# Performance work log

Measured on AMD Instinct MI355X. Metric: run time of the kernel, lower is better.

The kernel has to match this reference:

```python
import jax, jax.numpy as jnp
import numpy as np

DIM = 2048
DIM_HEAD = 128
HEADS = 16
FF_INNER = 4 * DIM  # 8192
ATTN_INNER = DIM_HEAD * HEADS  # 2048
FUSED_DIMS = (ATTN_INNER, DIM_HEAD, DIM_HEAD, FF_INNER * 2)
R = 8
B, N = 2, 2048


def setup_inputs() -> dict:
    key = jax.random.key(0)
    ks = jax.random.split(key, 12)
    s = 0.02
    return {
        "x": jax.random.normal(ks[0], (B, N, DIM), jnp.float32),
        "gamma": jnp.ones((DIM,), jnp.float32),
        "w_fused": jax.random.normal(ks[1], (DIM, sum(FUSED_DIMS)), jnp.float32) * s,
        "w_attn_out": jax.random.normal(ks[2], (ATTN_INNER, DIM), jnp.float32) * s,
        "w_ff_out": jax.random.normal(ks[3], (FF_INNER, DIM), jnp.float32) * s,
        "a_q": jax.random.normal(ks[4], (DIM, R), jnp.float32) * s,
        "b_q": jax.random.normal(ks[5], (R, ATTN_INNER), jnp.float32) * s,
        "a_k": jax.random.normal(ks[6], (DIM, R), jnp.float32) * s,
        "b_k": jax.random.normal(ks[7], (R, DIM_HEAD), jnp.float32) * s,
        "a_v": jax.random.normal(ks[8], (DIM, R), jnp.float32) * s,
        "b_v": jax.random.normal(ks[9], (R, DIM_HEAD), jnp.float32) * s,
        "a_o": jax.random.normal(ks[10], (ATTN_INNER, R), jnp.float32) * s,
        "b_o": jax.random.normal(ks[11], (R, DIM), jnp.float32) * s,
    }


def _rotate_half(t):
    t1, t2 = jnp.split(t, 2, axis=-1)
    return jnp.concatenate((-t2, t1), axis=-1)


def _rope(pos, t):
    return t * jnp.cos(pos) + _rotate_half(t) * jnp.sin(pos)


def reference(x, gamma, w_fused, w_attn_out, w_ff_out,
              a_q, b_q, a_k, b_k, a_v, b_v, a_o, b_o):
    b, n, d = x.shape
    # LayerNorm (beta buffer is zeros)
    mu = jnp.mean(x, -1, keepdims=True)
    var = jnp.var(x, -1, keepdims=True)
    xn = (x - mu) * jax.lax.rsqrt(var + 1e-5) * gamma

    proj = xn @ w_fused
    splits = np.cumsum(FUSED_DIMS)[:-1]
    q, k, v, ff = jnp.split(proj, splits, axis=-1)

    # fused QKV LoRA (scale alpha/r = 1)
    q = q + (xn @ a_q) @ b_q
    k = k + (xn @ a_k) @ b_k
    v = v + (xn @ a_v) @ b_v

    q = q.reshape(b, n, HEADS, DIM_HEAD).transpose(0, 2, 1, 3)  # b h n d
    q = q * (DIM_HEAD ** -0.5)

    # rotary embedding
    inv_freq = 1.0 / (10000.0 ** (jnp.arange(0, DIM_HEAD, 2, dtype=jnp.float32) / DIM_HEAD))
    freqs = jnp.arange(n, dtype=jnp.float32)[:, None] * inv_freq[None, :]  # n, d/2
    pos = jnp.concatenate((freqs, freqs), axis=-1)  # n, d
    q = _rope(pos, q)          # broadcast over b,h
    k = _rope(pos, k)          # b n d (single head, MQA)

    sim = jnp.einsum('bhid,bjd->bhij', q, k)
    causal = jnp.triu(jnp.ones((n, n), dtype=bool), 1)
    sim = jnp.where(causal, -jnp.finfo(sim.dtype).max, sim)
    attn = jax.nn.softmax(sim, axis=-1)
    out = jnp.einsum('bhij,bjd->bhid', attn, v)
    out = out.transpose(0, 2, 1, 3).reshape(b, n, ATTN_INNER)

    attn_out = out @ w_attn_out + (out @ a_o) @ b_o

    x1, gate = jnp.split(ff, 2, axis=-1)
    ff_out = (jax.nn.silu(gate) * x1) @ w_ff_out
    return attn_out + ff_out
```

## Files before the change

### kernel.cpp

```cpp
#include <hip/hip_runtime.h>

typedef unsigned short u16;
typedef __attribute__((ext_vector_type(8))) short s8v;
typedef __attribute__((ext_vector_type(4))) short s4v;
typedef __attribute__((ext_vector_type(4))) float f32x4;

__device__ __forceinline__ u16 f2bf(float f) {
  unsigned int u = __float_as_uint(f);
  u += ((u >> 16) & 1u) + 0x7FFFu;
  return (u16)(u >> 16);
}
__device__ __forceinline__ float bf2f(u16 h) {
  return __uint_as_float(((unsigned int)h) << 16);
}
__device__ __forceinline__ void gl_lds16(const void* g, void* l) {
  __builtin_amdgcn_global_load_lds(
      (__attribute__((address_space(1))) void*)g,
      (__attribute__((address_space(3))) void*)l, 16, 0, 0);
}
__device__ __forceinline__ f32x4 mfma16(s8v a, s8v b, f32x4 c) {
  return __builtin_amdgcn_mfma_f32_16x16x32_bf16(a, b, c, 0, 0, 0);
}

__global__ void transpose_cvt(const float* __restrict__ in, u16* __restrict__ out,
                              int rows, int cols, int ldo) {
  __shared__ float tile[32][33];
  int c0 = blockIdx.x * 32, r0 = blockIdx.y * 32;
  int tx = threadIdx.x, ty = threadIdx.y;
#pragma unroll
  for (int i = 0; i < 4; i++)
    tile[ty + i * 8][tx] = in[(long)(r0 + ty + i * 8) * cols + c0 + tx];
  __syncthreads();
#pragma unroll
  for (int i = 0; i < 4; i++)
    out[(long)(c0 + ty + i * 8) * ldo + r0 + tx] = f2bf(tile[tx][ty + i * 8]);
}

__global__ void vtrans(const u16* __restrict__ proj, u16* __restrict__ v_t) {
  __shared__ u16 tile[32][33];
  int n0 = blockIdx.x * 32, d0 = blockIdx.y * 32, b = blockIdx.z;
  int tx = threadIdx.x, ty = threadIdx.y;
#pragma unroll
  for (int i = 0; i < 4; i++)
    tile[ty + i * 8][tx] =
        proj[((long)b * 2048 + n0 + ty + i * 8) * 18688 + 2176 + d0 + tx];
  __syncthreads();
#pragma unroll
  for (int i = 0; i < 4; i++)
    v_t[((long)b * 128 + d0 + ty + i * 8) * 2048 + n0 + tx] = tile[tx][ty + i * 8];
}

__global__ void fill_aug_k(u16* __restrict__ wt, int N, int ldo, int naug,
                           const float* __restrict__ bq, const float* __restrict__ bk,
                           const float* __restrict__ bv) {
  long idx = (long)blockIdx.x * 256 + threadIdx.x;
  if (idx >= (long)N * naug) return;
  int n = (int)(idx / naug), j = (int)(idx % naug);
  float v = 0.f;
  if (bq && j < 8 && n < 2048) v = bq[j * 2048 + n];
  else if (bk && j >= 8 && j < 16 && n >= 2048 && n < 2176) v = bk[(j - 8) * 128 + (n - 2048)];
  else if (bv && j >= 16 && j < 24 && n >= 2176 && n < 2304) v = bv[(j - 16) * 128 + (n - 2176)];
  wt[(long)n * ldo + 2048 + j] = f2bf(v);
}

__global__ __launch_bounds__(256) void layernorm_k(const float* __restrict__ x,
                                                   const float* __restrict__ gamma,
                                                   u16* __restrict__ xn) {
  const int row = blockIdx.x, tid = threadIdx.x;
  const float* xr = x + (long)row * 2048 + tid * 8;
  float4 v0 = *(const float4*)xr;
  float4 v1 = *(const float4*)(xr + 4);
  float vals[8] = {v0.x, v0.y, v0.z, v0.w, v1.x, v1.y, v1.z, v1.w};
  float s = 0.f, q = 0.f;
#pragma unroll
  for (int e = 0; e < 8; e++) { s += vals[e]; q += vals[e] * vals[e]; }
#pragma unroll
  for (int off = 32; off > 0; off >>= 1) {
    s += __shfl_down(s, off, 64);
    q += __shfl_down(q, off, 64);
  }
  __shared__ float red[8];
  const int w = tid >> 6, lane = tid & 63;
  if (lane == 0) { red[w] = s; red[4 + w] = q; }
  __syncthreads();
  if (tid == 0) {
    float S = red[0] + red[1] + red[2] + red[3];
    float Q = red[4] + red[5] + red[6] + red[7];
    float mu = S * (1.f / 2048.f);
    float var = Q * (1.f / 2048.f) - mu * mu;
    red[0] = mu; red[1] = rsqrtf(var + 1e-5f);
  }
  __syncthreads();
  float mu = red[0], rs = red[1];
  const float* g = gamma + tid * 8;
  u16 ov[8];
#pragma unroll
  for (int e = 0; e < 8; e++) ov[e] = f2bf((vals[e] - mu) * rs * g[e]);
  *(s8v*)(xn + (long)row * 2112 + tid * 8) = *(const s8v*)ov;
}

__global__ __launch_bounds__(256) void lora_down_x(u16* __restrict__ xn_aug,
                                                   const float* __restrict__ aq,
                                                   const float* __restrict__ ak,
                                                   const float* __restrict__ av) {
  const int row = blockIdx.x, tid = threadIdx.x;
  s8v xv = *(const s8v*)(xn_aug + (long)row * 2112 + tid * 8);
  float acc[3][8];
#pragma unroll
  for (int m = 0; m < 3; m++)
#pragma unroll
    for (int j = 0; j < 8; j++) acc[m][j] = 0.f;
  const float* mats[3] = {aq, ak, av};
#pragma unroll
  for (int e = 0; e < 8; e++) {
    float xe = bf2f((u16)xv[e]);
    int k = tid * 8 + e;
#pragma unroll
    for (int m = 0; m < 3; m++) {
      const float4* ap = (const float4*)(mats[m] + (long)k * 8);
      float4 a0 = ap[0], a1 = ap[1];
      acc[m][0] += xe * a0.x; acc[m][1] += xe * a0.y;
      acc[m][2] += xe * a0.z; acc[m][3] += xe * a0.w;
      acc[m][4] += xe * a1.x; acc[m][5] += xe * a1.y;
      acc[m][6] += xe * a1.z; acc[m][7] += xe * a1.w;
    }
  }
#pragma unroll
  for (int m = 0; m < 3; m++)
#pragma unroll
    for (int j = 0; j < 8; j++)
#pragma unroll
      for (int off = 32; off > 0; off >>= 1)
        acc[m][j] += __shfl_down(acc[m][j], off, 64);
  __shared__ float red[4][24];
  const int w = tid >> 6, lane = tid & 63;
  if (lane == 0)
    for (int m = 0; m < 3; m++)
      for (int j = 0; j < 8; j++) red[w][m * 8 + j] = acc[m][j];
  __syncthreads();
  if (tid < 64) {
    float v = 0.f;
    if (tid < 24) v = red[0][tid] + red[1][tid] + red[2][tid] + red[3][tid];
    xn_aug[(long)row * 2112 + 2048 + tid] = f2bf(v);
  }
}

__global__ __launch_bounds__(256) void lora_down_ctx(u16* __restrict__ ctx_aug,
                                                     const float* __restrict__ ao) {
  const int row = blockIdx.x, tid = threadIdx.x;
  s8v xv = *(const s8v*)(ctx_aug + (long)row * 2080 + tid * 8);
  float acc[8];
#pragma unroll
  for (int j = 0; j < 8; j++) acc[j] = 0.f;
#pragma unroll
  for (int e = 0; e < 8; e++) {
    float xe = bf2f((u16)xv[e]);
    int k = tid * 8 + e;
    const float4* ap = (const float4*)(ao + (long)k * 8);
    float4 a0 = ap[0], a1 = ap[1];
    acc[0] += xe * a0.x; acc[1] += xe * a0.y; acc[2] += xe * a0.z; acc[3] += xe * a0.w;
    acc[4] += xe * a1.x; acc[5] += xe * a1.y; acc[6] += xe * a1.z; acc[7] += xe * a1.w;
  }
#pragma unroll
  for (int j = 0; j < 8; j++)
#pragma unroll
    for (int off = 32; off > 0; off >>= 1)
      acc[j] += __shfl_down(acc[j], off, 64);
  __shared__ float red[4][8];
  const int w = tid >> 6, lane = tid & 63;
  if (lane == 0)
    for (int j = 0; j < 8; j++) red[w][j] = acc[j];
  __syncthreads();
  if (tid < 32) {
    float v = 0.f;
    if (tid < 8) v = red[0][tid] + red[1][tid] + red[2][tid] + red[3][tid];
    ctx_aug[(long)row * 2080 + 2048 + tid] = f2bf(v);
  }
}

__global__ void rope_k(u16* __restrict__ proj) {
  int idx = blockIdx.x * 256 + threadIdx.x;
  int i = idx & 63;
  int u = (idx >> 6) % 17;
  int row = idx / (17 * 64);
  int n = row & 2047;
  float invf = __powf(10000.f, -(float)i * (1.f / 64.f));
  float ang = (float)n * invf;
  float cs = cosf(ang), sn = sinf(ang);
  int cb = (u < 16) ? u * 128 : 2048;
  u16* p = proj + (long)row * 18688 + cb + i;
  float t1 = bf2f(p[0]), t2 = bf2f(p[64]);
  float sc = (u < 16) ? 0.08838834764831845f : 1.f;
  p[0]  = f2bf((t1 * cs - t2 * sn) * sc);
  p[64] = f2bf((t2 * cs + t1 * sn) * sc);
}

__global__ void silu_mul_k(u16* __restrict__ proj) {
  long idx = (long)blockIdx.x * 256 + threadIdx.x;
  int row = (int)(idx >> 10);
  int c8 = (int)(idx & 1023) * 8;
  u16* px = proj + (long)row * 18688 + 2304 + c8;
  const u16* pg = proj + (long)row * 18688 + 10496 + c8;
  s8v xv = *(const s8v*)px;
  s8v gv = *(const s8v*)pg;
  u16 ov[8];
#pragma unroll
  for (int e = 0; e < 8; e++) {
    float x1 = bf2f((u16)xv[e]);
    float g = bf2f((u16)gv[e]);
    ov[e] = f2bf(x1 * g / (1.f + __expf(-g)));
  }
  *(s8v*)px = *(const s8v*)ov;
}

__global__ __launch_bounds__(512, 2) void gemm256_bt(const u16* __restrict__ A,
                                                     const u16* __restrict__ Bt,
                                                     u16* __restrict__ C) {
  __shared__ u16 sh[4 * 16384];
  const int cpx = gridDim.x >> 3;
  const int swz = (blockIdx.x & 7) * cpx + (blockIdx.x >> 3);
  const int bm = swz & 15;
  const int bn = swz >> 4;
  const int tid = threadIdx.x;
  const int w = tid >> 6, lane = tid & 63;
  const int quad = lane >> 4, l15 = lane & 15;
  const int wm = w >> 2, wn = w & 3;
  const int rseg = (quad ^ ((l15 >> 1) & 3)) * 8;
  const int aoff = (wm * 128 + l15) * 32 + rseg;
  const int boff = (wn * 64 + l15) * 32 + rseg;
  const int srow = lane >> 2;
  const int sseg = ((lane & 3) ^ ((lane >> 3) & 3)) * 8;
  const u16* aSrc = A + (long)(bm * 256 + w * 16 + srow) * 2112 + sseg;
  const u16* bSrc = Bt + (long)(bn * 256 + w * 16 + srow) * 2112 + sseg;

  f32x4 acc[8][4];
#pragma unroll
  for (int i = 0; i < 8; i++)
#pragma unroll
    for (int j = 0; j < 4; j++) acc[i][j] = {0.f, 0.f, 0.f, 0.f};

#pragma unroll
  for (int t = 0; t < 3; t++) {
    gl_lds16(aSrc + t * 32, sh + t * 16384 + w * 512);
    gl_lds16(bSrc + t * 32, sh + t * 16384 + 8192 + w * 512);
    gl_lds16(aSrc + 128L * 2112 + t * 32, sh + t * 16384 + 4096 + w * 512);
    gl_lds16(bSrc + 128L * 2112 + t * 32, sh + t * 16384 + 8192 + 4096 + w * 512);
  }
  asm volatile("s_waitcnt vmcnt(8)" ::: "memory");
  __builtin_amdgcn_s_barrier();

  s8v bf[4];
  int kcol = 96;

#define STAGE_UNIT(NB, MH)                                                    \
  gl_lds16(aSrc + (MH) * (128L * 2112) + kcol,                                \
           sh + (NB) * 16384 + (MH) * 4096 + w * 512);                        \
  gl_lds16(bSrc + (MH) * (128L * 2112) + kcol,                                \
           sh + (NB) * 16384 + 8192 + (MH) * 4096 + w * 512);

#define PHASE(CUR, MH, DOB, STG, VM)                                          \
  {                                                                           \
    const u16* Ab = sh + (CUR) * 16384 + aoff + (MH) * 2048;                  \
    s8v af0 = *(const s8v*)(Ab);                                              \
    s8v af1 = *(const s8v*)(Ab + 512);                                        \
    s8v af2 = *(const s8v*)(Ab + 1024);                                       \
    s8v af3 = *(const s8v*)(Ab + 1536);                                       \
    if (DOB) {                                                                \
      const u16* Bb = sh + (CUR) * 16384 + 8192 + boff;                       \
      bf[0] = *(const s8v*)(Bb);                                              \
      bf[1] = *(const s8v*)(Bb + 512);                                        \
      bf[2] = *(const s8v*)(Bb + 1024);                                       \
      bf[3] = *(const s8v*)(Bb + 1536);                                       \
    }                                                                         \
    if (STG) { STAGE_UNIT((((CUR) + 3) & 3), MH) }                            \
    __builtin_amdgcn_s_setprio(1);                                            \
    _Pragma("unroll") for (int ni = 0; ni < 4; ni++) {                        \
      acc[(MH) * 4 + 0][ni] = mfma16(bf[ni], af0, acc[(MH) * 4 + 0][ni]);     \
      acc[(MH) * 4 + 1][ni] = mfma16(bf[ni], af1, acc[(MH) * 4 + 1][ni]);     \
      acc[(MH) * 4 + 2][ni] = mfma16(bf[ni], af2, acc[(MH) * 4 + 2][ni]);     \
      acc[(MH) * 4 + 3][ni] = mfma16(bf[ni], af3, acc[(MH) * 4 + 3][ni]);     \
    }                                                                         \
    __builtin_amdgcn_s_setprio(0);                                            \
    if ((VM) == 8) asm volatile("s_waitcnt vmcnt(8)" ::: "memory");           \
    if ((VM) == 4) asm volatile("s_waitcnt vmcnt(4)" ::: "memory");           \
    if ((VM) == 0) asm volatile("s_waitcnt vmcnt(0)" ::: "memory");           \
    if ((VM) != -1) __builtin_amdgcn_s_barrier();                             \
  }

#define TILE(CUR, STG, VM)       \
  PHASE(CUR, 0, 1, STG, -1)      \
  PHASE(CUR, 1, 0, STG, VM)      \
  kcol += 32;

  for (int t4 = 0; t4 < 15; t4++) {
    TILE(0, 1, 8)
    TILE(1, 1, 8)
    TILE(2, 1, 8)
    TILE(3, 1, 8)
  }
  TILE(0, 1, 8)
  TILE(1, 1, 8)
  TILE(2, 1, 8)
  TILE(3, 0, 4)
  TILE(0, 0, 0)
  TILE(1, 0, -1)

#undef TILE
#undef PHASE
#undef STAGE_UNIT

  const long m0 = (long)bm * 256 + wm * 128;
  const long n0 = (long)bn * 256 + wn * 64;
#pragma unroll
  for (int mi = 0; mi < 8; mi++) {
    long row = m0 + mi * 16 + l15;
#pragma unroll
    for (int ni = 0; ni < 4; ni++) {
      long col = n0 + ni * 16 + quad * 4;
      s4v pk = {(short)f2bf(acc[mi][ni][0]), (short)f2bf(acc[mi][ni][1]),
                (short)f2bf(acc[mi][ni][2]), (short)f2bf(acc[mi][ni][3])};
      *(s4v*)(C + row * 18688 + col) = pk;
    }
  }
}

enum { STORE_F32 = 1, ADD_F32 = 2 };
template <int MODE>
__global__ __launch_bounds__(512, 1) void gemm_out(const u16* __restrict__ A, int lda,
                                                   const u16* __restrict__ Bt, int ldb,
                                                   float* __restrict__ Cv, int ldc, int K) {
  __shared__ u16 sh[4 * 12288];
  const int cpx = gridDim.x >> 3;
  const int swz = (blockIdx.x & 7) * cpx + (blockIdx.x >> 3);
  const int bm = swz & 31;
  const int bn = swz >> 5;
  const int tid = threadIdx.x;
  const int w = tid >> 6, lane = tid & 63;
  const int quad = lane >> 4, l15 = lane & 15;
  const int wm = w >> 2, wn = w & 3;
  const int rseg = (quad ^ ((l15 >> 1) & 3)) * 8;
  const int aoff = (wm * 64 + l15) * 32 + rseg;
  const int boff = 4096 + (wn * 64 + l15) * 32 + rseg;
  const int srow = lane >> 2;
  const int sseg = ((lane & 3) ^ ((lane >> 3) & 3)) * 8;
  const u16* aSrc = A + (long)(bm * 128 + w * 16 + srow) * lda + sseg;
  const u16* bSrc0 = Bt + (long)(bn * 256 + w * 16 + srow) * ldb + sseg;
  const u16* bSrc1 = Bt + (long)(bn * 256 + 128 + w * 16 + srow) * ldb + sseg;
  const int NT = K >> 5;

  f32x4 acc[4][4];
#pragma unroll
  for (int i = 0; i < 4; i++)
#pragma unroll
    for (int j = 0; j < 4; j++) acc[i][j] = {0.f, 0.f, 0.f, 0.f};

#pragma unroll
  for (int t = 0; t < 3; t++) {
    gl_lds16(aSrc + t * 32, sh + t * 12288 + w * 512);
    gl_lds16(bSrc0 + t * 32, sh + t * 12288 + 4096 + w * 512);
    gl_lds16(bSrc1 + t * 32, sh + t * 12288 + 8192 + w * 512);
  }
  asm volatile("s_waitcnt vmcnt(6)" ::: "memory");
  __builtin_amdgcn_s_barrier();

  int kcol = 96;
  for (int t = 0; t < NT; ++t) {
    const int cur = (t & 3) * 12288;
    const u16* Ab = sh + cur + aoff;
    const u16* Bb = sh + cur + boff;
    s8v af[4], bf[4];
#pragma unroll
    for (int mi = 0; mi < 4; mi++) af[mi] = *(const s8v*)(Ab + mi * 512);
#pragma unroll
    for (int ni = 0; ni < 4; ni++) bf[ni] = *(const s8v*)(Bb + ni * 512);
    if (t < NT - 3) {
      const int nb = ((t + 3) & 3) * 12288;
      gl_lds16(aSrc + kcol, sh + nb + w * 512);
      gl_lds16(bSrc0 + kcol, sh + nb + 4096 + w * 512);
      gl_lds16(bSrc1 + kcol, sh + nb + 8192 + w * 512);
      kcol += 32;
    }
    __builtin_amdgcn_s_setprio(1);
#pragma unroll
    for (int mi = 0; mi < 4; mi++)
#pragma unroll
      for (int ni = 0; ni < 4; ni++)
        acc[mi][ni] = mfma16(bf[ni], af[mi], acc[mi][ni]);
    __builtin_amdgcn_s_setprio(0);
    if (t < NT - 3)       asm volatile("s_waitcnt vmcnt(6)" ::: "memory");
    else if (t == NT - 3) asm volatile("s_waitcnt vmcnt(3)" ::: "memory");
    else if (t == NT - 2) asm volatile("s_waitcnt vmcnt(0)" ::: "memory");
    if (t != NT - 1) __builtin_amdgcn_s_barrier();
  }

  const long m0 = (long)bm * 128 + wm * 64;
  const long n0 = (long)bn * 256 + wn * 64;
#pragma unroll
  for (int mi = 0; mi < 4; mi++) {
    long row = m0 + mi * 16 + l15;
#pragma unroll
    for (int ni = 0; ni < 4; ni++) {
      long col = n0 + ni * 16 + quad * 4;
      float* p = Cv + row * ldc + col;
      if (MODE == STORE_F32) {
        *(f32x4*)p = acc[mi][ni];
      } else {
        f32x4 old = *(const f32x4*)p;
        old += acc[mi][ni];
        *(f32x4*)p = old;
      }
    }
  }
}

__global__ __launch_bounds__(256) void flash_k(const u16* __restrict__ proj,
                                               const u16* __restrict__ v_t,
                                               u16* __restrict__ ctx) {
  __shared__ u16 Kt[4 * 1024];
  __shared__ u16 Vx[8 * 512];
  __shared__ u16 Pw[4 * 512];
  const int qt = blockIdx.x, h = blockIdx.y, b = blockIdx.z;
  const int tid = threadIdx.x;
  const int w = tid >> 6, lane = tid & 63, quad = lane >> 4, l15 = lane & 15;
  const int qbase = qt * 64 + w * 16;

  s8v qf[4];
  {
    long rowQ = (long)b * 2048 + qbase + l15;
    const u16* qp = proj + rowQ * 18688 + h * 128 + quad * 8;
#pragma unroll
    for (int kk = 0; kk < 4; kk++) qf[kk] = *(const s8v*)(qp + kk * 32);
  }
  f32x4 o[8];
#pragma unroll
  for (int i = 0; i < 8; i++) o[i] = {0.f, 0.f, 0.f, 0.f};
  float m_i[4] = {-1e30f, -1e30f, -1e30f, -1e30f};
  float l_i[4] = {0.f, 0.f, 0.f, 0.f};

  const int srow = lane >> 2;
  const int sseg = ((lane & 3) ^ ((lane >> 3) & 3)) * 8;
  const int rseg = (quad ^ ((l15 >> 1) & 3)) * 8;

  const int nkb = 2 * qt + 2;
  for (int kb = 0; kb < nkb; kb++) {
    const int k0 = kb * 32;
    {
      long rK = (long)b * 2048 + k0;
#pragma unroll
      for (int h2 = 0; h2 < 2; h2++)
        gl_lds16(proj + (rK + h2 * 16 + srow) * 18688 + 2048 + w * 32 + sseg,
                 Kt + w * 1024 + h2 * 512);
#pragma unroll
      for (int h2 = 0; h2 < 2; h2++)
        gl_lds16(v_t + ((long)b * 128 + w * 32 + h2 * 16 + srow) * 2048 + k0 + sseg,
                 Vx + (w * 2 + h2) * 512);
    }
    __syncthreads();
    if (k0 <= qbase + 15) {
      f32x4 s[2];
#pragma unroll
      for (int ni = 0; ni < 2; ni++) {
        f32x4 a = {0.f, 0.f, 0.f, 0.f};
#pragma unroll
        for (int kk = 0; kk < 4; kk++) {
          s8v kf = *(const s8v*)(Kt + kk * 1024 + (ni * 16 + l15) * 32 + rseg);
          a = mfma16(qf[kk], kf, a);
        }
        s[ni] = a;
      }
#pragma unroll
      for (int ni = 0; ni < 2; ni++) {
        int kg = k0 + ni * 16 + l15;
#pragma unroll
        for (int r = 0; r < 4; r++)
          if (kg > qbase + quad * 4 + r) s[ni][r] = -1e30f;
      }
      float al[4];
#pragma unroll
      for (int r = 0; r < 4; r++) {
        float mx = fmaxf(s[0][r], s[1][r]);
#pragma unroll
        for (int off = 8; off > 0; off >>= 1)
          mx = fmaxf(mx, __shfl_xor(mx, off, 16));
        float mn = fmaxf(m_i[r], mx);
        al[r] = __expf(m_i[r] - mn);
        m_i[r] = mn;
      }
#pragma unroll
      for (int ni = 0; ni < 2; ni++)
#pragma unroll
        for (int r = 0; r < 4; r++) s[ni][r] = __expf(s[ni][r] - m_i[r]);
#pragma unroll
      for (int r = 0; r < 4; r++) {
        float rs = s[0][r] + s[1][r];
#pragma unroll
        for (int off = 8; off > 0; off >>= 1)
          rs += __shfl_xor(rs, off, 16);
        l_i[r] = l_i[r] * al[r] + rs;
      }
#pragma unroll
      for (int ni = 0; ni < 2; ni++)
#pragma unroll
        for (int r = 0; r < 4; r++) {
          int p = quad * 4 + r;
          int sg = ni * 2 + (l15 >> 3);
          int sp = sg ^ ((p >> 1) & 3);
          Pw[w * 512 + p * 32 + sp * 8 + (l15 & 7)] = f2bf(s[ni][r]);
        }
      __asm__ volatile("s_waitcnt lgkmcnt(0)" ::: "memory");
#pragma unroll
      for (int nt = 0; nt < 8; nt++)
#pragma unroll
        for (int r = 0; r < 4; r++) o[nt][r] *= al[r];
      s8v pf = *(const s8v*)(Pw + w * 512 + l15 * 32 + rseg);
#pragma unroll
      for (int nt = 0; nt < 8; nt++) {
        s8v vf = *(const s8v*)(Vx + (nt * 16 + l15) * 32 + rseg);
        o[nt] = mfma16(pf, vf, o[nt]);
      }
    }
    __syncthreads();
  }
  float inv[4];
#pragma unroll
  for (int r = 0; r < 4; r++) inv[r] = 1.f / l_i[r];
#pragma unroll
  for (int nt = 0; nt < 8; nt++)
#pragma unroll
    for (int r = 0; r < 4; r++) {
      long row = (long)b * 2048 + qbase + quad * 4 + r;
      ctx[row * 2080 + h * 128 + nt * 16 + l15] = f2bf(o[nt][r] * inv[r]);
    }
}

#define OFF_WF   0L
#define OFF_WO   78938112L
#define OFF_WFF  87457792L
#define OFF_XN   121012224L
#define OFF_PROJ 138313728L
#define WS_NEED  291405824L

extern "C" void kernel_launch(void* const* d_in, const int* in_sizes, int n_in,
                              void* d_out, int out_size, void* d_ws, size_t ws_size,
                              hipStream_t stream) {
  const float* x       = (const float*)d_in[0];
  const float* gamma   = (const float*)d_in[1];
  const float* w_fused = (const float*)d_in[2];
  const float* w_attn  = (const float*)d_in[3];
  const float* w_ff    = (const float*)d_in[4];
  const float* a_q = (const float*)d_in[5];
  const float* b_q = (const float*)d_in[6];
  const float* a_k = (const float*)d_in[7];
  const float* b_k = (const float*)d_in[8];
  const float* a_v = (const float*)d_in[9];
  const float* b_v = (const float*)d_in[10];
  const float* a_o = (const float*)d_in[11];
  const float* b_o = (const float*)d_in[12];
  float* out = (float*)d_out;
  if (ws_size < (size_t)WS_NEED) return;

  char* ws = (char*)d_ws;
  u16* wf_t    = (u16*)(ws + OFF_WF);
  u16* ctx_aug = (u16*)(ws + OFF_WF);
  u16* wo_t    = (u16*)(ws + OFF_WO);
  u16* wff_t   = (u16*)(ws + OFF_WFF);
  u16* xn_aug  = (u16*)(ws + OFF_XN);
  u16* v_t     = (u16*)(ws + OFF_XN);
  u16* proj    = (u16*)(ws + OFF_PROJ);

  dim3 tb(32, 8);
  transpose_cvt<<<dim3(18688 / 32, 2048 / 32), tb, 0, stream>>>(w_fused, wf_t, 2048, 18688, 2112);
  transpose_cvt<<<dim3(2048 / 32, 2048 / 32), tb, 0, stream>>>(w_attn, wo_t, 2048, 2048, 2080);
  transpose_cvt<<<dim3(2048 / 32, 8192 / 32), tb, 0, stream>>>(w_ff, wff_t, 8192, 2048, 8192);
  fill_aug_k<<<(18688 * 64 + 255) / 256, 256, 0, stream>>>(wf_t, 18688, 2112, 64, b_q, b_k, b_v);
  fill_aug_k<<<(2048 * 32 + 255) / 256, 256, 0, stream>>>(wo_t, 2048, 2080, 32, b_o, nullptr, nullptr);

  layernorm_k<<<4096, 256, 0, stream>>>(x, gamma, xn_aug);
  lora_down_x<<<4096, 256, 0, stream>>>(xn_aug, a_q, a_k, a_v);

  gemm256_bt<<<dim3(16 * (18688 / 256)), 512, 0, stream>>>(xn_aug, wf_t, proj);

  rope_k<<<(4096 * 17 * 64) / 256, 256, 0, stream>>>(proj);
  silu_mul_k<<<(4096 * 1024) / 256, 256, 0, stream>>>(proj);
  vtrans<<<dim3(64, 4, 2), tb, 0, stream>>>(proj, v_t);

  flash_k<<<dim3(32, 16, 2), 256, 0, stream>>>(proj, v_t, ctx_aug);
  lora_down_ctx<<<4096, 256, 0, stream>>>(ctx_aug, a_o);

  gemm_out<STORE_F32><<<dim3(256), 512, 0, stream>>>(
      ctx_aug, 2080, wo_t, 2080, out, 2048, 2080);
  gemm_out<ADD_F32><<<dim3(256), 512, 0, stream>>>(
      proj + 2304, 18688, wff_t, 8192, out, 2048, 8192);
}
```

Baseline: 1.315 ms.

## Software-pipeline LDS fragment loads across k-tiles with double-buffered B registers

Restructures the main GEMM loop so the A fragments and B fragments for the next k-tile are read from LDS during the current tile's second MFMA half, using ping-pong B register buffers. It removes the mid-tile barrier point and changes the vmcnt waits to one barrier per tile with a deeper wait, so LDS read latency is hidden behind MFMA work. This raises register pressure and tightens the hazard window between the LDS buffer being refilled and being read. Correctness depends on the revised waitcnt and barrier placement.

```diff
diff --git a/kernel.cpp b/kernel.cpp
--- a/kernel.cpp
+++ b/kernel.cpp
@@ -246,68 +246,90 @@
     gl_lds16(aSrc + 128L * 2112 + t * 32, sh + t * 16384 + 4096 + w * 512);
     gl_lds16(bSrc + 128L * 2112 + t * 32, sh + t * 16384 + 8192 + 4096 + w * 512);
   }
-  asm volatile("s_waitcnt vmcnt(8)" ::: "memory");
+  asm volatile("s_waitcnt vmcnt(4)" ::: "memory");
   __builtin_amdgcn_s_barrier();
 
-  s8v bf[4];
+  s8v afc[4], afn[4], bfA[4], bfB[4];
+  {
+    const u16* Ab0 = sh + aoff;
+    afc[0] = *(const s8v*)(Ab0);
+    afc[1] = *(const s8v*)(Ab0 + 512);
+    afc[2] = *(const s8v*)(Ab0 + 1024);
+    afc[3] = *(const s8v*)(Ab0 + 1536);
+    const u16* Bb0 = sh + 8192 + boff;
+    bfA[0] = *(const s8v*)(Bb0);
+    bfA[1] = *(const s8v*)(Bb0 + 512);
+    bfA[2] = *(const s8v*)(Bb0 + 1024);
+    bfA[3] = *(const s8v*)(Bb0 + 1536);
+  }
+
   int kcol = 96;
 
-#define STAGE_UNIT(NB, MH)                                                    \
+#define STAGE_U(NB, MH)                                                       \
   gl_lds16(aSrc + (MH) * (128L * 2112) + kcol,                                \
            sh + (NB) * 16384 + (MH) * 4096 + w * 512);                        \
   gl_lds16(bSrc + (MH) * (128L * 2112) + kcol,                                \
            sh + (NB) * 16384 + 8192 + (MH) * 4096 + w * 512);
 
-#define PHASE(CUR, MH, DOB, STG, VM)                                          \
-  {                                                                           \
-    const u16* Ab = sh + (CUR) * 16384 + aoff + (MH) * 2048;                  \
-    s8v af0 = *(const s8v*)(Ab);                                              \
-    s8v af1 = *(const s8v*)(Ab + 512);                                        \
-    s8v af2 = *(const s8v*)(Ab + 1024);                                       \
-    s8v af3 = *(const s8v*)(Ab + 1536);                                       \
-    if (DOB) {                                                                \
-      const u16* Bb = sh + (CUR) * 16384 + 8192 + boff;                       \
-      bf[0] = *(const s8v*)(Bb);                                              \
-      bf[1] = *(const s8v*)(Bb + 512);                                        \
-      bf[2] = *(const s8v*)(Bb + 1024);                                       \
-      bf[3] = *(const s8v*)(Bb + 1536);                                       \
-    }                                                                         \
-    if (STG) { STAGE_UNIT((((CUR) + 3) & 3), MH) }                            \
+#define TILE(CUR, BFC, BFN, STG, RA, VM)                                      \
+  {                \
+    const u16* Abn = sh + (CUR) * 16384 + aoff + 2048;                        \
+    afn[0] = *(const s8v*)(Abn);                                              \
+    afn[1] = *(const s8v*)(Abn + 512);                                        \
+    afn[2] = *(const s8v*)(Abn + 1024);                                       \
+    afn[3] = *(const s8v*)(Abn + 1536);                                       \
+    if (STG) { STAGE_U((((CUR) + 3) & 3), 0) }                                \
     __builtin_amdgcn_s_setprio(1);                                            \
     _Pragma("unroll") for (int ni = 0; ni < 4; ni++) {                        \
-      acc[(MH) * 4 + 0][ni] = mfma16(bf[ni], af0, acc[(MH) * 4 + 0][ni]);     \
-      acc[(MH) * 4 + 1][ni] = mfma16(bf[ni], af1, acc[(MH) * 4 + 1][ni]);     \
-      acc[(MH) * 4 + 2][ni] = mfma16(bf[ni], af2, acc[(MH) * 4 + 2][ni]);     \
-      acc[(MH) * 4 + 3][ni] = mfma16(bf[ni], af3, acc[(MH) * 4 + 3][ni]);     \
+      acc[0][ni] = mfma16(BFC[ni], afc[0], acc[0][ni]);                       \
+      acc[1][ni] = mfma16(BFC[ni], afc[1], acc[1][ni]);                       \
+      acc[2][ni] = mfma16(BFC[ni], afc[2], acc[2][ni]);                       \
+      acc[3][ni] = mfma16(BFC[ni], afc[3], acc[3][ni]);                       \
     }                                                                         \
     __builtin_amdgcn_s_setprio(0);                                            \
-    if ((VM) == 8) asm volatile("s_waitcnt vmcnt(8)" ::: "memory");           \
+       \
+    if (RA) {                                                                 \
+      const u16* Abc = sh + (((CUR) + 1) & 3) * 16384 + aoff;                 \
+      afc[0] = *(const s8v*)(Abc);                                            \
+      afc[1] = *(const s8v*)(Abc + 512);                                      \
+      afc[2] = *(const s8v*)(Abc + 1024);                                     \
+      afc[3] = *(const s8v*)(Abc + 1536);                                     \
+      const u16* Bbn = sh + (((CUR) + 1) & 3) * 16384 + 8192 + boff;          \
+      BFN[0] = *(const s8v*)(Bbn);                                            \
+      BFN[1] = *(const s8v*)(Bbn + 512);                                      \
+      BFN[2] = *(const s8v*)(Bbn + 1024);                                     \
+      BFN[3] = *(const s8v*)(Bbn + 1536);                                     \
+    }                                                                         \
+    if (STG) { STAGE_U((((CUR) + 3) & 3), 1) }                                \
+    __builtin_amdgcn_s_setprio(1);                                            \
+    _Pragma("unroll") for (int ni = 0; ni < 4; ni++) {                        \
+      acc[4][ni] = mfma16(BFC[ni], afn[0], acc[4][ni]);                       \
+      acc[5][ni] = mfma16(BFC[ni], afn[1], acc[5][ni]);                       \
+      acc[6][ni] = mfma16(BFC[ni], afn[2], acc[6][ni]);                       \
+      acc[7][ni] = mfma16(BFC[ni], afn[3], acc[7][ni]);                       \
+    }                                                                         \
+    __builtin_amdgcn_s_setprio(0);                                            \
     if ((VM) == 4) asm volatile("s_waitcnt vmcnt(4)" ::: "memory");           \
     if ((VM) == 0) asm volatile("s_waitcnt vmcnt(0)" ::: "memory");           \
     if ((VM) != -1) __builtin_amdgcn_s_barrier();                             \
-  }
-
-#define TILE(CUR, STG, VM)       \
-  PHASE(CUR, 0, 1, STG, -1)      \
-  PHASE(CUR, 1, 0, STG, VM)      \
+  }                                                                           \
   kcol += 32;
 
   for (int t4 = 0; t4 < 15; t4++) {
-    TILE(0, 1, 8)
-    TILE(1, 1, 8)
-    TILE(2, 1, 8)
-    TILE(3, 1, 8)
-  }
-  TILE(0, 1, 8)
-  TILE(1, 1, 8)
-  TILE(2, 1, 8)
-  TILE(3, 0, 4)
-  TILE(0, 0, 0)
-  TILE(1, 0, -1)
+    TILE(0, bfA, bfB, 1, 1, 4)
+    TILE(1, bfB, bfA, 1, 1, 4)
+    TILE(2, bfA, bfB, 1, 1, 4)
+    TILE(3, bfB, bfA, 1, 1, 4)
+  }
+  TILE(0, bfA, bfB, 1, 1, 4)
+  TILE(1, bfB, bfA, 1, 1, 4)
+  TILE(2, bfA, bfB, 1, 1, 4)
+  TILE(3, bfB, bfA, 0, 1, 0)
+  TILE(0, bfA, bfB, 0, 1, -1)
+  TILE(1, bfB, bfA, 0, 0, -1)
 
 #undef TILE
-#undef PHASE
-#undef STAGE_UNIT
+#undef STAGE_U
 
   const long m0 = (long)bm * 256 + wm * 128;
   const long n0 = (long)bn * 256 + wn * 64;
```

After: 1.373 ms. +4.4%, slower.
